# Kernel tuning notes

Measured on AMD Instinct MI355X. Metric: run time of the kernel, lower is better.

Reference implementation:

```python
import jax, jax.numpy as jnp
import numpy as np

D_EMBED = 1024
N_HEADS = 16
BATCH = 2
SEQ = 2048


def setup_inputs() -> dict:
    key = jax.random.key(0)
    k1, k2, k3 = jax.random.split(key, 3)
    scale = 0.02
    x = jax.random.normal(k1, (BATCH, SEQ, D_EMBED), dtype=jnp.float32)
    w_qkv = jax.random.normal(k2, (D_EMBED, 3 * D_EMBED), dtype=jnp.float32) * scale
    b_qkv = jnp.zeros((3 * D_EMBED,), dtype=jnp.float32)
    w_o = jax.random.normal(k3, (D_EMBED, D_EMBED), dtype=jnp.float32) * scale
    b_o = jnp.zeros((D_EMBED,), dtype=jnp.float32)
    return {"x": x, "w_qkv": w_qkv, "b_qkv": b_qkv, "w_o": w_o, "b_o": b_o}


def reference(x, w_qkv, b_qkv, w_o, b_o):
    bs, sl, ed = x.shape
    nh = N_HEADS
    hd = ed // nh
    # fused QKV projection, split into q, k, v
    qkv = x @ w_qkv + b_qkv                      # [bs, sl, 3*ed]
    q, k, v = jnp.split(qkv, 3, axis=2)
    # [bs, sl, (nh hd)] -> [bs, nh, sl, hd]
    def heads(t):
        return t.reshape(bs, sl, nh, hd).transpose(0, 2, 1, 3)
    q, k, v = heads(q), heads(k), heads(v)
    # scaled dot-product attention with causal mask (full SxS scores, as in the original)
    scores = jnp.einsum('bhqd,bhkd->bhqk', q, k) / jnp.sqrt(jnp.float32(hd))
    causal = jnp.tril(jnp.ones((sl, sl), dtype=bool))
    scores = jnp.where(causal[None, None, :, :], scores, jnp.float32(-jnp.inf))
    attn = jax.nn.softmax(scores, axis=-1)       # dropout p=0 -> identity
    out = jnp.einsum('bhqk,bhkd->bhqd', attn, v) # [bs, nh, sl, hd]
    out = out.transpose(0, 2, 1, 3).reshape(bs, sl, ed)
    return out @ w_o + b_o
```

## Files before the change

### kernel.cpp

```cpp
#include <hip/hip_runtime.h>
#include <hip/hip_bf16.h>

typedef __hip_bfloat16 bf16;
typedef unsigned short u16;
typedef __attribute__((ext_vector_type(8))) short short8;
typedef __attribute__((ext_vector_type(4))) float floatx4;

#define D_EMBED 1024
#define N_HEADS 16
#define HEAD_DIM 64
#define BATCH 2
#define SEQ 2048
#define ROWS (BATCH * SEQ)
#define QKV_COLS (3 * D_EMBED)
#define QSCALE 0.1803368801f

__device__ __forceinline__ void g2l16(const void* g, void* l) {
    __builtin_amdgcn_global_load_lds(
        (const __attribute__((address_space(1))) unsigned int*)g,
        (__attribute__((address_space(3))) unsigned int*)l,
        16, 0, 0);
}

__device__ __forceinline__ u16 f2b_bits(float f) {
    bf16 h = __float2bfloat16(f);
    u16 u;
    __builtin_memcpy(&u, &h, 2);
    return u;
}

__device__ __forceinline__ unsigned pack2(float a, float b) {
    return (unsigned)f2b_bits(a) | ((unsigned)f2b_bits(b) << 16);
}

__device__ __forceinline__ float fexp2(float x) {
#if __has_builtin(__builtin_amdgcn_exp2f)
    return __builtin_amdgcn_exp2f(x);
#else
    return exp2f(x);
#endif
}

__device__ __forceinline__ unsigned permpack(float a, float b) {
#if __has_builtin(__builtin_amdgcn_perm)
    return __builtin_amdgcn_perm(__float_as_uint(b), __float_as_uint(a), 0x07060302u);
#else
    return (__float_as_uint(a) >> 16) | (__float_as_uint(b) & 0xFFFF0000u);
#endif
}

__global__ __launch_bounds__(256)
void prep(const float* __restrict__ x, const float* __restrict__ w_qkv,
          const float* __restrict__ w_o, bf16* __restrict__ xb,
          bf16* __restrict__ wqkvT, bf16* __restrict__ woT)
{
    __shared__ u16 T[64][72];
    const int tid = threadIdx.x;
    const int bid = blockIdx.x;

    if (bid < 4096) {
        const int i = bid * 256 + tid;
        const float4 v = reinterpret_cast<const float4*>(x)[i];
        ushort4 o;
        o.x = f2b_bits(v.x); o.y = f2b_bits(v.y);
        o.z = f2b_bits(v.z); o.w = f2b_bits(v.w);
        reinterpret_cast<ushort4*>(xb)[i] = o;
        return;
    }
    const float* in; u16* out; int R, C, bx, by;
    if (bid < 4864) {
        const int t = bid - 4096;
        in = w_qkv; out = reinterpret_cast<u16*>(wqkvT); R = 1024; C = 3072;
        bx = t % 48; by = t / 48;
    } else {
        const int t = bid - 4864;
        in = w_o; out = reinterpret_cast<u16*>(woT); R = 1024; C = 1024;
        bx = t % 16; by = t / 16;
    }
    const int r0 = by * 64, c0 = bx * 64;
#pragma unroll
    for (int it = 0; it < 4; ++it) {
        const int r = (tid >> 4) + it * 16;
        const int c4 = (tid & 15) * 4;
        const float4 v = *reinterpret_cast<const float4*>(in + (size_t)(r0 + r) * C + c0 + c4);
        T[c4 + 0][r] = f2b_bits(v.x);
        T[c4 + 1][r] = f2b_bits(v.y);
        T[c4 + 2][r] = f2b_bits(v.z);
        T[c4 + 3][r] = f2b_bits(v.w);
    }
    __syncthreads();
#pragma unroll
    for (int it = 0; it < 4; ++it) {
        const int rr = (tid >> 4) + it * 16;
        const int cc4 = (tid & 15) * 4;
        ushort4 o = *reinterpret_cast<const ushort4*>(&T[rr][cc4]);
        *reinterpret_cast<ushort4*>(out + (size_t)(c0 + rr) * R + r0 + cc4) = o;
    }
}

__global__ __launch_bounds__(256)
void gemm_qkv(const bf16* __restrict__ A, const bf16* __restrict__ Bt,
              const float* __restrict__ bias,
              bf16* __restrict__ qb, bf16* __restrict__ kb, bf16* __restrict__ vtb)
{
    __shared__ __align__(16) char smem[32768];
    char* BUF0 = smem;
    char* BUF1 = smem + 16384;

    const int tid = threadIdx.x;
    const int lane = tid & 63, w = tid >> 6;
    const int quad = lane >> 4, l15 = lane & 15;
    const int mw = (w >> 1) * 64, nw = (w & 1) * 64;
    const int blockM = blockIdx.y * 128, blockN = blockIdx.x * 128;

    const int row0 = tid >> 2, ch = tid & 3;
    const int off0 = (tid & ~63) * 16;
    const bf16* Asrc0 = A + (size_t)(blockM + row0) * 1024 + ch * 8;
    const bf16* Asrc1 = Asrc0 + (size_t)64 * 1024;
    const bf16* Bsrc0 = Bt + (size_t)(blockN + row0) * 1024 + ch * 8;
    const bf16* Bsrc1 = Bsrc0 + (size_t)64 * 1024;

    auto stage = [&](int k0, char* buf) {
        g2l16(Asrc0 + k0, buf + off0);
        g2l16(Asrc1 + k0, buf + off0 + 4096);
        g2l16(Bsrc0 + k0, buf + 8192 + off0);
        g2l16(Bsrc1 + k0, buf + 8192 + off0 + 4096);
    };

    floatx4 acc[4][4];
#pragma unroll
    for (int i = 0; i < 4; ++i)
#pragma unroll
        for (int j = 0; j < 4; ++j) acc[i][j] = (floatx4){0.f, 0.f, 0.f, 0.f};

    auto compute = [&](char* buf) {
        short8 af[4], bfr[4];
#pragma unroll
        for (int mi = 0; mi < 4; ++mi)
            af[mi] = *reinterpret_cast<const short8*>(
                buf + (mw + mi * 16 + l15) * 64 + quad * 16);
#pragma unroll
        for (int ni = 0; ni < 4; ++ni)
            bfr[ni] = *reinterpret_cast<const short8*>(
                buf + 8192 + (nw + ni * 16 + l15) * 64 + quad * 16);
#pragma unroll
        for (int mi = 0; mi < 4; ++mi)
#pragma unroll
            for (int ni = 0; ni < 4; ++ni)
                acc[mi][ni] = __builtin_amdgcn_mfma_f32_16x16x32_bf16(
                    af[mi], bfr[ni], acc[mi][ni], 0, 0, 0);
    };

    stage(0, BUF0);
    __syncthreads();
#pragma unroll 1
    for (int k0 = 0; k0 < 1024; k0 += 64) {
        if (k0 + 32 < 1024) stage(k0 + 32, BUF1);
        compute(BUF0);
        __syncthreads();
        if (k0 + 64 < 1024) stage(k0 + 64, BUF0);
        compute(BUF1);
        __syncthreads();
    }

    u16* W = reinterpret_cast<u16*>(smem + w * 2304);
    const bool isq = (blockN < 1024);
    const bool isv = (blockN >= 2048);

    float bvn[4];
#pragma unroll
    for (int ni = 0; ni < 4; ++ni) bvn[ni] = bias[blockN + nw + ni * 16 + l15];

    if (!isv) {
        bf16* dstbuf = isq ? qb : kb;
        const int coloff = blockN - (isq ? 0 : 1024);
#pragma unroll
        for (int mi = 0; mi < 4; ++mi) {
#pragma unroll
            for (int ni = 0; ni < 4; ++ni) {
#pragma unroll
                for (int r = 0; r < 4; ++r) {
                    float val = acc[mi][ni][r] + bvn[ni];
                    if (isq) val *= QSCALE;
                    W[(quad * 4 + r) * 72 + ni * 16 + l15] = f2b_bits(val);
                }
            }
#pragma unroll
            for (int half = 0; half < 2; ++half) {
                const int idx = half * 64 + lane;
                const int rowL = idx >> 3, chh = idx & 7;
                short8 v = *reinterpret_cast<const short8*>(W + rowL * 72 + chh * 8);
                const int grow = blockM + mw + mi * 16 + rowL;
                const int gcol = coloff + nw + chh * 8;
                *reinterpret_cast<short8*>(
                    reinterpret_cast<u16*>(dstbuf) + (size_t)grow * 1024 + gcol) = v;
            }
        }
    } else {
        const int col0 = blockN - 2048 + nw;
        const int h = col0 >> 6;
        const int bh = (blockM >> 11) * 16 + h;
        const int sb = (blockM & 2047) + mw;
        u16* vdst = reinterpret_cast<u16*>(vtb) + (size_t)bh * 64 * SEQ;
#pragma unroll
        for (int mi = 0; mi < 4; ++mi) {
#pragma unroll
            for (int ni = 0; ni < 4; ++ni) {
#pragma unroll
                for (int r = 0; r < 4; ++r)
                    W[(quad * 4 + r) * 72 + ni * 16 + l15] =
                        f2b_bits(acc[mi][ni][r] + bvn[ni]);
            }
#pragma unroll
            for (int mc = 0; mc < 2; ++mc) {
                u16 tmp[8];
#pragma unroll
                for (int e = 0; e < 8; ++e) tmp[e] = W[(mc * 8 + e) * 72 + lane];
                const int s = sb + mi * 16 + mc * 8;
                *reinterpret_cast<short8*>(vdst + (size_t)lane * SEQ + s) =
                    *reinterpret_cast<const short8*>(tmp);
            }
        }
    }
}

__global__ __launch_bounds__(256)
void gemm_out(const bf16* __restrict__ A, const bf16* __restrict__ Bt,
              const float* __restrict__ bias, float* __restrict__ outf)
{
    __shared__ __align__(16) char smem[24576];
    char* BUF0 = smem;
    char* BUF1 = smem + 12288;

    const int tid = threadIdx.x;
    const int lane = tid & 63, w = tid >> 6;
    const int quad = lane >> 4, l15 = lane & 15;
    const int mw = (w >> 1) * 64, nw = (w & 1) * 32;
    const int blockM = blockIdx.y * 128, blockN = blockIdx.x * 64;

    const int row0 = tid >> 2, ch = tid & 3;
    const int off0 = (tid & ~63) * 16;
    const bf16* Asrc0 = A + (size_t)(blockM + row0) * 1024 + ch * 8;
    const bf16* Asrc1 = Asrc0 + (size_t)64 * 1024;
    const bf16* Bsrc0 = Bt + (size_t)(blockN + row0) * 1024 + ch * 8;

    auto stage = [&](int k0, char* buf) {
        g2l16(Asrc0 + k0, buf + off0);
        g2l16(Asrc1 + k0, buf + off0 + 4096);
        g2l16(Bsrc0 + k0, buf + 8192 + off0);
    };

    floatx4 acc[4][2];
#pragma unroll
    for (int i = 0; i < 4; ++i)
#pragma unroll
        for (int j = 0; j < 2; ++j) acc[i][j] = (floatx4){0.f, 0.f, 0.f, 0.f};

    auto compute = [&](char* buf) {
        short8 af[4], bfr[2];
#pragma unroll
        for (int mi = 0; mi < 4; ++mi)
            af[mi] = *reinterpret_cast<const short8*>(
                buf + (mw + mi * 16 + l15) * 64 + quad * 16);
#pragma unroll
        for (int ni = 0; ni < 2; ++ni)
            bfr[ni] = *reinterpret_cast<const short8*>(
                buf + 8192 + (nw + ni * 16 + l15) * 64 + quad * 16);
#pragma unroll
        for (int mi = 0; mi < 4; ++mi)
#pragma unroll
            for (int ni = 0; ni < 2; ++ni)
                acc[mi][ni] = __builtin_amdgcn_mfma_f32_16x16x32_bf16(
                    af[mi], bfr[ni], acc[mi][ni], 0, 0, 0);
    };

    stage(0, BUF0);
    __syncthreads();
#pragma unroll 1
    for (int k0 = 0; k0 < 1024; k0 += 64) {
        if (k0 + 32 < 1024) stage(k0 + 32, BUF1);
        compute(BUF0);
        __syncthreads();
        if (k0 + 64 < 1024) stage(k0 + 64, BUF0);
        compute(BUF1);
        __syncthreads();
    }

    float bvn[2];
#pragma unroll
    for (int ni = 0; ni < 2; ++ni) bvn[ni] = bias[blockN + nw + ni * 16 + l15];

#pragma unroll
    for (int mi = 0; mi < 4; ++mi)
#pragma unroll
        for (int r = 0; r < 4; ++r) {
            const int row = blockM + mw + mi * 16 + quad * 4 + r;
#pragma unroll
            for (int ni = 0; ni < 2; ++ni) {
                const int col = blockN + nw + ni * 16 + l15;
                outf[(size_t)row * 1024 + col] = acc[mi][ni][r] + bvn[ni];
            }
        }
}

__global__ __launch_bounds__(256)
void attn_mfma(const bf16* __restrict__ qb, const bf16* __restrict__ kb,
               const bf16* __restrict__ vtb, bf16* __restrict__ ob)
{
    __shared__ __align__(16) char smem[40960];
    char* KV0 = smem;
    char* KV1 = smem + 16384;
    const int tid = threadIdx.x;
    const int lane = tid & 63, w = tid >> 6;
    const int quad = lane >> 4, l15 = lane & 15;
    char* Ps = smem + 32768 + w * 2048;

    const int pi = blockIdx.x;
    const int bh = blockIdx.y;
    const int b = bh >> 4, h = bh & 15;

    const int qtS = pi, qtB = 31 - pi;
    const int q0S = qtS * 64, q0B = qtB * 64;
    const int KT = qtB + 1;
    const int qrowS = q0S + w * 16 + l15;
    const int qrowB = q0B + w * 16 + l15;

    const size_t kvrow = (size_t)b * SEQ;
    const size_t vbase = (size_t)bh * 64 * SEQ;

    const short8 ones = {0x3F80, 0x3F80, 0x3F80, 0x3F80,
                         0x3F80, 0x3F80, 0x3F80, 0x3F80};

    const int row0 = tid >> 3;
    const int lch = (tid & 7) ^ (row0 & 7);
    const int loff0 = (tid & ~63) * 16;
    const int loff1 = loff0 + 4096;
    const bf16* ksrc0 = kb + (kvrow + row0) * D_EMBED + h * 64 + lch * 8;
    const bf16* ksrc1 = ksrc0 + (size_t)32 * D_EMBED;
    const bf16* vsrc0 = vtb + vbase + (size_t)row0 * SEQ + lch * 8;
    const bf16* vsrc1 = vsrc0 + (size_t)32 * SEQ;

    {
        const bf16* qsrcS = qb + (kvrow + q0S + row0) * D_EMBED + h * 64 + lch * 8;
        const bf16* qsrcB = qb + (kvrow + q0B + row0) * D_EMBED + h * 64 + lch * 8;
        g2l16(qsrcS, KV1 + loff0);
        g2l16(qsrcS + (size_t)32 * D_EMBED, KV1 + loff1);
        g2l16(qsrcB, KV1 + 8192 + loff0);
        g2l16(qsrcB + (size_t)32 * D_EMBED, KV1 + 8192 + loff1);
        g2l16(ksrc0, KV0 + loff0);
        g2l16(ksrc1, KV0 + loff1);
        g2l16(vsrc0, KV0 + 8192 + loff0);
        g2l16(vsrc1, KV0 + 8192 + loff1);
    }
    __syncthreads();

    const int qoff = (w * 16 + l15) * 128;
    const int x0 = (quad ^ (l15 & 7)) * 16;
    const int x1 = ((quad + 4) ^ (l15 & 7)) * 16;
    const short8 qS0 = *reinterpret_cast<const short8*>(KV1 + qoff + x0);
    const short8 qS1 = *reinterpret_cast<const short8*>(KV1 + qoff + x1);
    const short8 qB0 = *reinterpret_cast<const short8*>(KV1 + 8192 + qoff + x0);
    const short8 qB1 = *reinterpret_cast<const short8*>(KV1 + 8192 + qoff + x1);
    __syncthreads();

    floatx4 OaccS[4], OaccB[4], LaccS, LaccB;
#pragma unroll
    for (int i = 0; i < 4; ++i) {
        OaccS[i] = (floatx4){0.f, 0.f, 0.f, 0.f};
        OaccB[i] = (floatx4){0.f, 0.f, 0.f, 0.f};
    }
    LaccS = (floatx4){0.f, 0.f, 0.f, 0.f};
    LaccB = (floatx4){0.f, 0.f, 0.f, 0.f};

    auto prefetch = [&](int nkt, char* dst) {
        const size_t ko = (size_t)nkt * 64;
        g2l16(ksrc0 + ko * D_EMBED, dst + loff0);
        g2l16(ksrc1 + ko * D_EMBED, dst + loff1);
        g2l16(vsrc0 + ko, dst + 8192 + loff0);
        g2l16(vsrc1 + ko, dst + 8192 + loff1);
    };

    auto compute = [&](int kt, char* Ks, char* Vs) {
        const int k0 = kt * 64;
        short8 kf[2][4], vf[2][4];
#pragma unroll
        for (int ms = 0; ms < 4; ++ms) {
            const int roff = (ms * 16 + l15) * 128;
            kf[0][ms] = *reinterpret_cast<const short8*>(Ks + roff + x0);
            kf[1][ms] = *reinterpret_cast<const short8*>(Ks + roff + x1);
        }
#pragma unroll
        for (int ks = 0; ks < 2; ++ks)
#pragma unroll
            for (int ds = 0; ds < 4; ++ds)
                vf[ks][ds] = *reinterpret_cast<const short8*>(
                    Vs + (ds * 16 + l15) * 128 + (((quad + ks * 4) ^ (l15 & 7)) * 16));

        {
            floatx4 S[4];
#pragma unroll
            for (int ms = 0; ms < 4; ++ms) {
                floatx4 t = (floatx4){0.f, 0.f, 0.f, 0.f};
                t = __builtin_amdgcn_mfma_f32_16x16x32_bf16(kf[0][ms], qB0, t, 0, 0, 0);
                S[ms] = __builtin_amdgcn_mfma_f32_16x16x32_bf16(kf[1][ms], qB1, t, 0, 0, 0);
            }
            const bool diag = (kt == KT - 1);
#pragma unroll
            for (int ms = 0; ms < 4; ++ms) {
                float p[4];
#pragma unroll
                for (int r = 0; r < 4; ++r) {
                    float s = S[ms][r];
                    if (diag && (k0 + ms * 16 + quad * 4 + r) > qrowB) s = -1e30f;
                    p[r] = fexp2(s);
                }
                const int k = ms * 16 + quad * 4;
                uint2 pw;
                pw.x = permpack(p[0], p[1]);
                pw.y = permpack(p[2], p[3]);
                *reinterpret_cast<uint2*>(Ps + (k >> 3) * 256 + l15 * 16 + (k & 7) * 2) = pw;
            }
#pragma unroll
            for (int ks = 0; ks < 2; ++ks) {
                const short8 pf = *reinterpret_cast<const short8*>(
                    Ps + (ks * 4 + quad) * 256 + l15 * 16);
                LaccB = __builtin_amdgcn_mfma_f32_16x16x32_bf16(ones, pf, LaccB, 0, 0, 0);
#pragma unroll
                for (int ds = 0; ds < 4; ++ds)
                    OaccB[ds] = __builtin_amdgcn_mfma_f32_16x16x32_bf16(
                        vf[ks][ds], pf, OaccB[ds], 0, 0, 0);
            }
        }

        if (kt <= qtS) {
            floatx4 S[4];
#pragma unroll
            for (int ms = 0; ms < 4; ++ms) {
                floatx4 t = (floatx4){0.f, 0.f, 0.f, 0.f};
                t = __builtin_amdgcn_mfma_f32_16x16x32_bf16(kf[0][ms], qS0, t, 0, 0, 0);
                S[ms] = __builtin_amdgcn_mfma_f32_16x16x32_bf16(kf[1][ms], qS1, t, 0, 0, 0);
            }
            const bool diag = (kt == qtS);
#pragma unroll
            for (int ms = 0; ms < 4; ++ms) {
                float p[4];
#pragma unroll
                for (int r = 0; r < 4; ++r) {
                    float s = S[ms][r];
                    if (diag && (k0 + ms * 16 + quad * 4 + r) > qrowS) s = -1e30f;
                    p[r] = fexp2(s);
                }
                const int k = ms * 16 + quad * 4;
                uint2 pw;
                pw.x = permpack(p[0], p[1]);
                pw.y = permpack(p[2], p[3]);
                *reinterpret_cast<uint2*>(Ps + (k >> 3) * 256 + l15 * 16 + (k & 7) * 2) = pw;
            }
#pragma unroll
            for (int ks = 0; ks < 2; ++ks) {
                const short8 pf = *reinterpret_cast<const short8*>(
                    Ps + (ks * 4 + quad) * 256 + l15 * 16);
                LaccS = __builtin_amdgcn_mfma_f32_16x16x32_bf16(ones, pf, LaccS, 0, 0, 0);
#pragma unroll
                for (int ds = 0; ds < 4; ++ds)
                    OaccS[ds] = __builtin_amdgcn_mfma_f32_16x16x32_bf16(
                        vf[ks][ds], pf, OaccS[ds], 0, 0, 0);
            }
        }
    };

#pragma unroll 1
    for (int kt = 0; kt < KT; kt += 2) {
        if (kt + 1 < KT) prefetch(kt + 1, KV1);
        compute(kt, KV0, KV0 + 8192);
        __syncthreads();
        if (kt + 1 >= KT) break;
        if (kt + 2 < KT) prefetch(kt + 2, KV0);
        compute(kt + 1, KV1, KV1 + 8192);
        __syncthreads();
    }

#pragma unroll
    for (int which = 0; which < 2; ++which) {
        const floatx4* Oacc = which ? OaccB : OaccS;
        const float invl = 1.f / (which ? LaccB[0] : LaccS[0]);
        const int q0 = which ? q0B : q0S;
#pragma unroll
        for (int ds = 0; ds < 4; ++ds) {
            const int d = ds * 16 + quad * 4;
            uint2 ow;
            ow.x = pack2(Oacc[ds][0] * invl, Oacc[ds][1] * invl);
            ow.y = pack2(Oacc[ds][2] * invl, Oacc[ds][3] * invl);
            *reinterpret_cast<uint2*>(
                Ps + (d >> 3) * 256 + l15 * 16 + (d & 7) * 2) = ow;
        }
#pragma unroll
        for (int it = 0; it < 2; ++it) {
            const int idx = it * 64 + lane;
            const int ch = idx >> 4, q = idx & 15;
            short8 ov = *reinterpret_cast<const short8*>(Ps + ch * 256 + q * 16);
            *reinterpret_cast<short8*>(
                ob + (kvrow + q0 + w * 16 + q) * D_EMBED + h * 64 + ch * 8) = ov;
        }
    }
}

extern "C" void kernel_launch(void* const* d_in, const int* in_sizes, int n_in,
                              void* d_out, int out_size, void* d_ws, size_t ws_size,
                              hipStream_t stream)
{
    const float* x     = (const float*)d_in[0];
    const float* w_qkv = (const float*)d_in[1];
    const float* b_qkv = (const float*)d_in[2];
    const float* w_o   = (const float*)d_in[3];
    const float* b_o   = (const float*)d_in[4];
    float* out = (float*)d_out;

    bf16* xb     = (bf16*)d_ws;
    bf16* wqkvT  = xb + (size_t)4096 * 1024;
    bf16* woT    = wqkvT + (size_t)3072 * 1024;
    bf16* qbuf   = woT + (size_t)1024 * 1024;
    bf16* kbuf   = qbuf + (size_t)4096 * 1024;
    bf16* vtb    = kbuf + (size_t)4096 * 1024;
    bf16* attnb  = vtb + (size_t)4096 * 1024;

    dim3 blk(256);

    prep<<<dim3(5120), blk, 0, stream>>>(x, w_qkv, w_o, xb, wqkvT, woT);

    gemm_qkv<<<dim3(24, 32), blk, 0, stream>>>(xb, wqkvT, b_qkv, qbuf, kbuf, vtb);

    attn_mfma<<<dim3(16, 32), blk, 0, stream>>>(qbuf, kbuf, vtb, attnb);

    gemm_out<<<dim3(16, 32), blk, 0, stream>>>(attnb, woT, b_o, out);
}
```

Measured before the change: 178.9 us.

## Interleave big/small query tile attention and remap blocks to a 1D grid

Computes the S-score MFMAs for both paired query tiles up front, uses separate P scratch buffers for each, and then issues both PV updates interleaved, so the two independent chains can overlap instead of running one after the other. The grid becomes 1D, with heads in the low bits and the pair index spread across slots so block scheduling order changes. This costs more LDS (48KB) and more live registers, which may lower occupancy.

```diff
diff --git a/kernel.cpp b/kernel.cpp
--- a/kernel.cpp
+++ b/kernel.cpp
@@ -307,16 +307,19 @@
 void attn_mfma(const bf16* __restrict__ qb, const bf16* __restrict__ kb,
                const bf16* __restrict__ vtb, bf16* __restrict__ ob)
 {
-    __shared__ __align__(16) char smem[40960];
+    __shared__ __align__(16) char smem[49152];
     char* KV0 = smem;
     char* KV1 = smem + 16384;
     const int tid = threadIdx.x;
     const int lane = tid & 63, w = tid >> 6;
     const int quad = lane >> 4, l15 = lane & 15;
-    char* Ps = smem + 32768 + w * 2048;
-
-    const int pi = blockIdx.x;
-    const int bh = blockIdx.y;
+    char* PsB = smem + 32768 + w * 2048;
+    char* PsS = smem + 40960 + w * 2048;
+
+    const int l = blockIdx.x;
+    const int bh = l & 31;
+    const int slot = l >> 5;
+    const int pi = (slot < 8) ? slot : 23 - slot;
     const int b = bh >> 4, h = bh & 15;
 
     const int qtS = pi, qtB = 31 - pi;
@@ -382,6 +385,7 @@
 
     auto compute = [&](int kt, char* Ks, char* Vs) {
         const int k0 = kt * 64;
+        const bool doS = (kt <= qtS);
         short8 kf[2][4], vf[2][4];
 #pragma unroll
         for (int ms = 0; ms < 4; ++ms) {
@@ -396,75 +400,74 @@
                 vf[ks][ds] = *reinterpret_cast<const short8*>(
                     Vs + (ds * 16 + l15) * 128 + (((quad + ks * 4) ^ (l15 & 7)) * 16));
 
-        {
-            floatx4 S[4];
+        floatx4 SB[4], SS[4];
+#pragma unroll
+        for (int ms = 0; ms < 4; ++ms) {
+            floatx4 t = (floatx4){0.f, 0.f, 0.f, 0.f};
+            t = __builtin_amdgcn_mfma_f32_16x16x32_bf16(kf[0][ms], qB0, t, 0, 0, 0);
+            SB[ms] = __builtin_amdgcn_mfma_f32_16x16x32_bf16(kf[1][ms], qB1, t, 0, 0, 0);
+        }
+        if (doS) {
 #pragma unroll
             for (int ms = 0; ms < 4; ++ms) {
                 floatx4 t = (floatx4){0.f, 0.f, 0.f, 0.f};
-                t = __builtin_amdgcn_mfma_f32_16x16x32_bf16(kf[0][ms], qB0, t, 0, 0, 0);
-                S[ms] = __builtin_amdgcn_mfma_f32_16x16x32_bf16(kf[1][ms], qB1, t, 0, 0, 0);
-            }
-            const bool diag = (kt == KT - 1);
+                t = __builtin_amdgcn_mfma_f32_16x16x32_bf16(kf[0][ms], qS0, t, 0, 0, 0);
+                SS[ms] = __builtin_amdgcn_mfma_f32_16x16x32_bf16(kf[1][ms], qS1, t, 0, 0, 0);
+            }
+        }
+
+        const bool diagB = (kt == KT - 1);
+#pragma unroll
+        for (int ms = 0; ms < 4; ++ms) {
+            float p[4];
+#pragma unroll
+            for (int r = 0; r < 4; ++r) {
+                float s = SB[ms][r];
+                if (diagB && (k0 + ms * 16 + quad * 4 + r) > qrowB) s = -1e30f;
+                p[r] = fexp2(s);
+            }
+            const int k = ms * 16 + quad * 4;
+            uint2 pw;
+            pw.x = permpack(p[0], p[1]);
+            pw.y = permpack(p[2], p[3]);
+            *reinterpret_cast<uint2*>(PsB + (k >> 3) * 256 + l15 * 16 + (k & 7) * 2) = pw;
+        }
+        if (doS) {
+            const bool diagS = (kt == qtS);
 #pragma unroll
             for (int ms = 0; ms < 4; ++ms) {
                 float p[4];
 #pragma unroll
                 for (int r = 0; r < 4; ++r) {
-                    float s = S[ms][r];
-                    if (diag && (k0 + ms * 16 + quad * 4 + r) > qrowB) s = -1e30f;
+                    float s = SS[ms][r];
+                    if (diagS && (k0 + ms * 16 + quad * 4 + r) > qrowS) s = -1e30f;
                     p[r] = fexp2(s);
                 }
                 const int k = ms * 16 + quad * 4;
                 uint2 pw;
                 pw.x = permpack(p[0], p[1]);
                 pw.y = permpack(p[2], p[3]);
-                *reinterpret_cast<uint2*>(Ps + (k >> 3) * 256 + l15 * 16 + (k & 7) * 2) = pw;
-            }
-#pragma unroll
-            for (int ks = 0; ks < 2; ++ks) {
-                const short8 pf = *reinterpret_cast<const short8*>(
-                    Ps + (ks * 4 + quad) * 256 + l15 * 16);
-                LaccB = __builtin_amdgcn_mfma_f32_16x16x32_bf16(ones, pf, LaccB, 0, 0, 0);
-#pragma unroll
-                for (int ds = 0; ds < 4; ++ds)
-                    OaccB[ds] = __builtin_amdgcn_mfma_f32_16x16x32_bf16(
-                        vf[ks][ds], pf, OaccB[ds], 0, 0, 0);
-            }
-        }
-
-        if (kt <= qtS) {
-            floatx4 S[4];
-#pragma unroll
-            for (int ms = 0; ms < 4; ++ms) {
-                floatx4 t = (floatx4){0.f, 0.f, 0.f, 0.f};
-                t = __builtin_amdgcn_mfma_f32_16x16x32_bf16(kf[0][ms], qS0, t, 0, 0, 0);
-                S[ms] = __builtin_amdgcn_mfma_f32_16x16x32_bf16(kf[1][ms], qS1, t, 0, 0, 0);
-            }
-            const bool diag = (kt == qtS);
-#pragma unroll
-            for (int ms = 0; ms < 4; ++ms) {
-                float p[4];
-#pragma unroll
-                for (int r = 0; r < 4; ++r) {
-                    float s = S[ms][r];
-                    if (diag && (k0 + ms * 16 + quad * 4 + r) > qrowS) s = -1e30f;
-                    p[r] = fexp2(s);
-                }
-                const int k = ms * 16 + quad * 4;
-                uint2 pw;
-                pw.x = permpack(p[0], p[1]);
-                pw.y = permpack(p[2], p[3]);
-                *reinterpret_cast<uint2*>(Ps + (k >> 3) * 256 + l15 * 16 + (k & 7) * 2) = pw;
-            }
-#pragma unroll
-            for (int ks = 0; ks < 2; ++ks) {
-                const short8 pf = *reinterpret_cast<const short8*>(
-                    Ps + (ks * 4 + quad) * 256 + l15 * 16);
-                LaccS = __builtin_amdgcn_mfma_f32_16x16x32_bf16(ones, pf, LaccS, 0, 0, 0);
+                *reinterpret_cast<uint2*>(PsS + (k >> 3) * 256 + l15 * 16 + (k & 7) * 2) = pw;
+            }
+        }
+
+#pragma unroll
+        for (int ks = 0; ks < 2; ++ks) {
+            const short8 pfB = *reinterpret_cast<const short8*>(
+                PsB + (ks * 4 + quad) * 256 + l15 * 16);
+            LaccB = __builtin_amdgcn_mfma_f32_16x16x32_bf16(ones, pfB, LaccB, 0, 0, 0);
+#pragma unroll
+            for (int ds = 0; ds < 4; ++ds)
+                OaccB[ds] = __builtin_amdgcn_mfma_f32_16x16x32_bf16(
+                    vf[ks][ds], pfB, OaccB[ds], 0, 0, 0);
+            if (doS) {
+                const short8 pfS = *reinterpret_cast<const short8*>(
+                    PsS + (ks * 4 + quad) * 256 + l15 * 16);
+                LaccS = __builtin_amdgcn_mfma_f32_16x16x32_bf16(ones, pfS, LaccS, 0, 0, 0);
 #pragma unroll
                 for (int ds = 0; ds < 4; ++ds)
                     OaccS[ds] = __builtin_amdgcn_mfma_f32_16x16x32_bf16(
-                        vf[ks][ds], pf, OaccS[ds], 0, 0, 0);
+                        vf[ks][ds], pfS, OaccS[ds], 0, 0, 0);
             }
         }
     };
@@ -492,15 +495,15 @@
             ow.x = pack2(Oacc[ds][0] * invl, Oacc[ds][1] * invl);
             ow.y = pack2(Oacc[ds][2] * invl, Oacc[ds][3] * invl);
             *reinterpret_cast<uint2*>(
-                Ps + (d >> 3) * 256 + l15 * 16 + (d & 7) * 2) = ow;
+                PsB + (d >> 3) * 256 + l15 * 16 + (d & 7) * 2) = ow;
         }
 #pragma unroll
         for (int it = 0; it < 2; ++it) {
             const int idx = it * 64 + lane;
-            const int ch = idx >> 4, q = idx & 15;
-            short8 ov = *reinterpret_cast<const short8*>(Ps + ch * 256 + q * 16);
+            const int chh = idx >> 4, q = idx & 15;
+            short8 ov = *reinterpret_cast<const short8*>(PsB + chh * 256 + q * 16);
             *reinterpret_cast<short8*>(
-                ob + (kvrow + q0 + w * 16 + q) * D_EMBED + h * 64 + ch * 8) = ov;
+                ob + (kvrow + q0 + w * 16 + q) * D_EMBED + h * 64 + chh * 8) = ov;
         }
     }
 }
@@ -530,7 +533,7 @@
 
     gemm_qkv<<<dim3(24, 32), blk, 0, stream>>>(xb, wqkvT, b_qkv, qbuf, kbuf, vtb);
 
-    attn_mfma<<<dim3(16, 32), blk, 0, stream>>>(qbuf, kbuf, vtb, attnb);
+    attn_mfma<<<dim3(512), blk, 0, stream>>>(qbuf, kbuf, vtb, attnb);
 
     gemm_out<<<dim3(16, 32), blk, 0, stream>>>(attnb, woT, b_o, out);
 }
```

Result: faster. 174.7 us (-2.3%).
